# Optimization experiments

Hardware: AMD Instinct MI355X
Metric: run time of the kernel (lower is better)

Reference implementation:

```python
import jax, jax.numpy as jnp
import numpy as np

HIDDEN = 2048
NUM_HEADS = 16
HEAD_DIM = HIDDEN // NUM_HEADS  # 128
SCALE = HEAD_DIM ** -0.5


def setup_inputs() -> dict:
    key = jax.random.key(0)
    ks = jax.random.split(key, 5)
    B, S = 2, 2048
    init = HIDDEN ** -0.5  # roughly kaiming-uniform scale for Linear weights
    return {
        "hidden_states": jax.random.normal(ks[0], (B, S, HIDDEN), dtype=jnp.float32),
        "Wq": jax.random.normal(ks[1], (HIDDEN, HIDDEN), dtype=jnp.float32) * init,
        "Wk": jax.random.normal(ks[2], (HIDDEN, HIDDEN), dtype=jnp.float32) * init,
        "Wv": jax.random.normal(ks[3], (HIDDEN, HIDDEN), dtype=jnp.float32) * init,
        "Wo": jax.random.normal(ks[4], (HIDDEN, HIDDEN), dtype=jnp.float32) * init,
    }


def reference(hidden_states, Wq, Wk, Wv, Wo):
    B, S, _ = hidden_states.shape
    # Projections (nn.Linear: x @ W.T; weights stored as [out, in])
    q = (hidden_states @ Wq.T).reshape(B, S, NUM_HEADS, HEAD_DIM).transpose(0, 2, 1, 3)
    k = (hidden_states @ Wk.T).reshape(B, S, NUM_HEADS, HEAD_DIM).transpose(0, 2, 1, 3)
    v = (hidden_states @ Wv.T).reshape(B, S, NUM_HEADS, HEAD_DIM).transpose(0, 2, 1, 3)
    # Full quadratic attention (faithful to the source's explicit materialization)
    scores = jnp.einsum("bhqd,bhkd->bhqk", q, k) * SCALE  # [B,H,S,S]
    probs = jax.nn.softmax(scores, axis=-1)
    attn = jnp.einsum("bhqk,bhkd->bhqd", probs, v)  # [B,H,S,Dh]
    attn = attn.transpose(0, 2, 1, 3).reshape(B, S, HIDDEN)
    return attn @ Wo.T
```

## Files before the change

### kernel.cpp

```cpp
#include <hip/hip_runtime.h>
#include <cstdint>

#define HIDDEN 2048
#define NHEADS 16
#define DH 128
#define BATCH 2
#define SEQ 2048
#define MTOT 4096
#define BH (BATCH * NHEADS)

typedef __attribute__((ext_vector_type(8))) short bf16x8;
typedef __attribute__((ext_vector_type(4))) float f32x4;

static constexpr float QSCALE = (float)(0.08838834764831845 * 1.4426950408889634);

__device__ __forceinline__ unsigned short f2bf(float f) {
  union { float f; uint32_t u; } v; v.f = f;
  uint32_t r = v.u + 0x7FFFu + ((v.u >> 16) & 1u);
  return (unsigned short)(r >> 16);
}
__device__ __forceinline__ uint32_t cvtpk(float lo, float hi) {
  uint32_t r;
  asm("v_cvt_pk_bf16_f32 %0, %1, %2" : "=v"(r) : "v"(lo), "v"(hi));
  return r;
}
__device__ __forceinline__ f32x4 mfma16(bf16x8 a, bf16x8 b, f32x4 c) {
  return __builtin_amdgcn_mfma_f32_16x16x32_bf16(a, b, c, 0, 0, 0);
}

typedef const __attribute__((address_space(1))) unsigned char* gas1_t;
typedef __attribute__((address_space(3))) unsigned char* las3_t;
__device__ __forceinline__ void gll16(const void* g, void* l) {
  __builtin_amdgcn_global_load_lds((gas1_t)g, (las3_t)l, 16, 0, 0);
}

__global__ __launch_bounds__(256) void cast_all(
    const float* __restrict__ X, const float* __restrict__ Wq,
    const float* __restrict__ Wk, const float* __restrict__ Wv,
    const float* __restrict__ Wo, unsigned short* __restrict__ Xb,
    unsigned short* __restrict__ Wqb, unsigned short* __restrict__ Wkb,
    unsigned short* __restrict__ Wvb, unsigned short* __restrict__ Wob) {
  const int n1 = MTOT * HIDDEN;
  const int i = (blockIdx.x * 256 + threadIdx.x) * 4;
  const float* s;
  unsigned short* d;
  int o;
  if (i < n1) {
    s = X; d = Xb; o = i;
  } else {
    const int j = i - n1;
    const int w = j >> 22;
    o = j & ((1 << 22) - 1);
    s = (w == 0) ? Wq : (w == 1) ? Wk : (w == 2) ? Wv : Wo;
    d = (w == 0) ? Wqb : (w == 1) ? Wkb : (w == 2) ? Wvb : Wob;
  }
  float4 f = *(const float4*)&s[o];
  ushort4 u;
  u.x = f2bf(f.x); u.y = f2bf(f.y); u.z = f2bf(f.z); u.w = f2bf(f.w);
  *(ushort4*)&d[o] = u;
}

template <int VM, bool PF>
__device__ __forceinline__ void pipe_body(
    int kt, char* SM, const unsigned short* aS0, const unsigned short* aS1,
    const unsigned short* bS0, const unsigned short* bS1,
    const unsigned short* bS2, const unsigned short* bS3, int wv, int wr,
    int wc, int g, int lr, f32x4 (&acc)[4][4]) {
  const char* Ac = SM + (kt % 3) * 49152;
  const char* Bc = Ac + 16384;
  char* slot2 = SM + ((kt + 2) % 3) * 49152;
  const size_t ko = (size_t)(kt + 2) * 64;
  const int rx = lr & 7;
  bf16x8 a0[4], b0[4], a1[4], b1[4];
#pragma unroll
  for (int mi = 0; mi < 4; ++mi)
    a0[mi] = *(const bf16x8*)(Ac + (wr * 64 + mi * 16 + lr) * 128 + ((g ^ rx) * 16));
#pragma unroll
  for (int ni = 0; ni < 4; ++ni)
    b0[ni] = *(const bf16x8*)(Bc + (wc * 64 + ni * 16 + lr) * 128 + ((g ^ rx) * 16));
  if (PF) {
    gll16(aS0 + ko, slot2 + wv * 2048);
    gll16(aS1 + ko, slot2 + wv * 2048 + 1024);
    gll16(bS0 + ko, slot2 + 16384 + wv * 4096);
    gll16(bS1 + ko, slot2 + 16384 + wv * 4096 + 1024);
    gll16(bS2 + ko, slot2 + 16384 + wv * 4096 + 2048);
    gll16(bS3 + ko, slot2 + 16384 + wv * 4096 + 3072);
  }
#pragma unroll
  for (int mi = 0; mi < 4; ++mi)
    a1[mi] = *(const bf16x8*)(Ac + (wr * 64 + mi * 16 + lr) * 128 + (((4 + g) ^ rx) * 16));
#pragma unroll
  for (int ni = 0; ni < 4; ++ni)
    b1[ni] = *(const bf16x8*)(Bc + (wc * 64 + ni * 16 + lr) * 128 + (((4 + g) ^ rx) * 16));
  __builtin_amdgcn_s_setprio(1);
#pragma unroll
  for (int mi = 0; mi < 4; ++mi)
#pragma unroll
    for (int ni = 0; ni < 4; ++ni)
      acc[mi][ni] = mfma16(a0[mi], b0[ni], acc[mi][ni]);
#pragma unroll
  for (int mi = 0; mi < 4; ++mi)
#pragma unroll
    for (int ni = 0; ni < 4; ++ni)
      acc[mi][ni] = mfma16(a1[mi], b1[ni], acc[mi][ni]);
  __builtin_amdgcn_s_setprio(0);
  if (VM == 6) asm volatile("s_waitcnt vmcnt(6)" ::: "memory");
  else if (VM == 0) asm volatile("s_waitcnt vmcnt(0)" ::: "memory");
  if (VM >= 0) __builtin_amdgcn_s_barrier();
}

#define PIPE_SETUP(Abase, Bbase)                                              \
  const int idxA0 = wv * 128 + lane, idxA1 = idxA0 + 64;                      \
  const int rA0 = idxA0 >> 3, cA0 = (idxA0 & 7) ^ (rA0 & 7);                  \
  const int rA1 = idxA1 >> 3, cA1 = (idxA1 & 7) ^ (rA1 & 7);                  \
  const unsigned short* aS0 = (Abase) + (size_t)(m0 + rA0) * HIDDEN + cA0 * 8;\
  const unsigned short* aS1 = (Abase) + (size_t)(m0 + rA1) * HIDDEN + cA1 * 8;\
  const int idxB0 = wv * 256 + lane, idxB1 = idxB0 + 64,                      \
            idxB2 = idxB0 + 128, idxB3 = idxB0 + 192;                         \
  const int rB0 = idxB0 >> 3, cB0 = (idxB0 & 7) ^ (rB0 & 7);                  \
  const int rB1 = idxB1 >> 3, cB1 = (idxB1 & 7) ^ (rB1 & 7);                  \
  const int rB2 = idxB2 >> 3, cB2 = (idxB2 & 7) ^ (rB2 & 7);                  \
  const int rB3 = idxB3 >> 3, cB3 = (idxB3 & 7) ^ (rB3 & 7);                  \
  const unsigned short* bS0 = (Bbase) + (size_t)(n0 + rB0) * HIDDEN + cB0 * 8;\
  const unsigned short* bS1 = (Bbase) + (size_t)(n0 + rB1) * HIDDEN + cB1 * 8;\
  const unsigned short* bS2 = (Bbase) + (size_t)(n0 + rB2) * HIDDEN + cB2 * 8;\
  const unsigned short* bS3 = (Bbase) + (size_t)(n0 + rB3) * HIDDEN + cB3 * 8;

#define PIPE_PROLOGUE()                                                       \
  _Pragma("unroll") for (int tt = 0; tt < 2; ++tt) {                          \
    char* slot = SM + tt * 49152;                                             \
    const size_t ko = (size_t)tt * 64;                                        \
    gll16(aS0 + ko, slot + wv * 2048);                                        \
    gll16(aS1 + ko, slot + wv * 2048 + 1024);                                 \
    gll16(bS0 + ko, slot + 16384 + wv * 4096);                                \
    gll16(bS1 + ko, slot + 16384 + wv * 4096 + 1024);                         \
    gll16(bS2 + ko, slot + 16384 + wv * 4096 + 2048);                         \
    gll16(bS3 + ko, slot + 16384 + wv * 4096 + 3072);                         \
  }                                                                           \
  asm volatile("s_waitcnt vmcnt(6)" ::: "memory");                            \
  __builtin_amdgcn_s_barrier();

#define PIPE_LOOP()                                                           \
  for (int kt = 0; kt < 30; ++kt)                                             \
    pipe_body<6, true>(kt, SM, aS0, aS1, bS0, bS1, bS2, bS3, wv, wr, wc, g,   \
                       lr, acc);                                              \
  pipe_body<0, false>(30, SM, aS0, aS1, bS0, bS1, bS2, bS3, wv, wr, wc, g,    \
                      lr, acc);                                               \
  pipe_body<-1, false>(31, SM, aS0, aS1, bS0, bS1, bS2, bS3, wv, wr, wc, g,   \
                       lr, acc);

__global__ __launch_bounds__(512) void gemm_qkv_pipe(
    const unsigned short* __restrict__ A, const unsigned short* __restrict__ Wq,
    const unsigned short* __restrict__ Wk, const unsigned short* __restrict__ Wv,
    unsigned short* __restrict__ Qb, unsigned short* __restrict__ Kb,
    unsigned short* __restrict__ Vb) {
  __shared__ __align__(16) char SM[147456];
  const int tid = threadIdx.x;
  const int lane = tid & 63, wv = tid >> 6;
  const int wr = wv >> 2, wc = wv & 3;
  const int g = lane >> 4, lr = lane & 15;
  const int which = blockIdx.x >> 3;
  const int m0 = blockIdx.y * 128, n0 = (blockIdx.x & 7) * 256;
  const unsigned short* W = (which == 0) ? Wq : (which == 1) ? Wk : Wv;

  PIPE_SETUP(A, W)

  f32x4 acc[4][4];
#pragma unroll
  for (int i = 0; i < 4; ++i)
#pragma unroll
    for (int j = 0; j < 4; ++j) acc[i][j] = (f32x4){0.f, 0.f, 0.f, 0.f};

  PIPE_PROLOGUE()
  PIPE_LOOP()

  const float alpha = (which == 0) ? QSCALE : 1.0f;
  unsigned short* C = (which == 0) ? Qb : (which == 1) ? Kb : Vb;
#pragma unroll
  for (int mi = 0; mi < 4; ++mi)
#pragma unroll
    for (int ni = 0; ni < 4; ++ni)
#pragma unroll
      for (int r = 0; r < 4; ++r) {
        const int row = m0 + wr * 64 + mi * 16 + g * 4 + r;
        const int col = n0 + wc * 64 + ni * 16 + lr;
        const unsigned short v = f2bf(acc[mi][ni][r] * alpha);
        const int b = row >> 11, s = row & (SEQ - 1);
        const int h = col >> 7, d = col & (DH - 1);
        const size_t base = (size_t)(b * NHEADS + h) * SEQ * DH;
        if (which == 0)
          C[base + (size_t)s * DH + d] = v;
        else if (which == 1)
          C[base + (size_t)(s >> 5) * 4096 + (d >> 3) * 256 + (s & 31) * 8 + (d & 7)] = v;
        else
          C[base + (size_t)(s >> 3) * 1024 + d * 8 + (s & 7)] = v;
      }
}

__global__ __launch_bounds__(512) void gemm_out_pipe(
    const unsigned short* __restrict__ A, const unsigned short* __restrict__ W,
    float* __restrict__ C) {
  __shared__ __align__(16) char SM[147456];
  const int tid = threadIdx.x;
  const int lane = tid & 63, wv = tid >> 6;
  const int wr = wv >> 2, wc = wv & 3;
  const int g = lane >> 4, lr = lane & 15;
  const int m0 = blockIdx.y * 128, n0 = blockIdx.x * 256;

  PIPE_SETUP(A, W)

  f32x4 acc[4][4];
#pragma unroll
  for (int i = 0; i < 4; ++i)
#pragma unroll
    for (int j = 0; j < 4; ++j) acc[i][j] = (f32x4){0.f, 0.f, 0.f, 0.f};

  PIPE_PROLOGUE()
  PIPE_LOOP()

#pragma unroll
  for (int mi = 0; mi < 4; ++mi)
#pragma unroll
    for (int ni = 0; ni < 4; ++ni)
#pragma unroll
      for (int r = 0; r < 4; ++r) {
        const int row = m0 + wr * 64 + mi * 16 + g * 4 + r;
        const int col = n0 + wc * 64 + ni * 16 + lr;
        C[(size_t)row * HIDDEN + col] = acc[mi][ni][r];
      }
}

__global__ __launch_bounds__(256, 3) void attn_mfma(const unsigned short* __restrict__ Q,
                                                    const unsigned short* __restrict__ K,
                                                    const unsigned short* __restrict__ V,
                                                    unsigned short* __restrict__ Ab) {
  const int bid = blockIdx.x;
  const int bh = bid & 31;
  const int q0 = (bid >> 5) * 128;
  const int tid = threadIdx.x;
  const int wv = tid >> 6, lane = tid & 63;
  const int g = lane >> 4, lr = lane & 15;
  const unsigned short* Qh = Q + (size_t)bh * SEQ * DH;
  const unsigned short* Kh = K + (size_t)bh * SEQ * DH;
  const unsigned short* Vh = V + (size_t)bh * SEQ * DH;

  __shared__ __align__(16) unsigned short Kls[3][4096];
  __shared__ __align__(16) unsigned short Vls[3][4096];
  __shared__ __align__(16) unsigned short Pw[4][16][40];

  bf16x8 qf[2][4];
#pragma unroll
  for (int m = 0; m < 2; ++m)
#pragma unroll
    for (int kb = 0; kb < 4; ++kb)
      qf[m][kb] = *(const bf16x8*)&Qh[(size_t)(q0 + wv * 32 + m * 16 + lr) * DH +
                                      kb * 32 + g * 8];

  f32x4 acc[2][8];
#pragma unroll
  for (int m = 0; m < 2; ++m)
#pragma unroll
    for (int dn = 0; dn < 8; ++dn) acc[m][dn] = (f32x4){0.f, 0.f, 0.f, 0.f};
  float mrun[2] = {-1e30f, -1e30f};
  float lrun[2] = {0.f, 0.f};

#pragma unroll
  for (int tt = 0; tt < 2; ++tt)
#pragma unroll
    for (int j = 0; j < 2; ++j) {
      const int c = j * 256 + tid;
      gll16(Kh + (size_t)tt * 4096 + c * 8, (char*)&Kls[tt][0] + j * 4096 + wv * 1024);
      gll16(Vh + (size_t)tt * 4096 + c * 8, (char*)&Vls[tt][0] + j * 4096 + wv * 1024);
    }

  for (int t = 0; t < 64; ++t) {
    const int cur = t % 3;
    asm volatile("s_waitcnt vmcnt(4)" ::: "memory");
    __builtin_amdgcn_s_barrier();
    if (t + 2 < 64) {
      const int nx = (t + 2) % 3;
      const unsigned short* Kn = Kh + (size_t)(t + 2) * 4096;
      const unsigned short* Vn = Vh + (size_t)(t + 2) * 4096;
      char* kd = (char*)&Kls[nx][0];
      char* vd = (char*)&Vls[nx][0];
#pragma unroll
      for (int j = 0; j < 2; ++j) {
        const int c = j * 256 + tid;
        gll16(Kn + (size_t)c * 8, kd + j * 4096 + wv * 1024);
        gll16(Vn + (size_t)c * 8, vd + j * 4096 + wv * 1024);
      }
    }

    const char* Kc = (const char*)&Kls[cur][0];
    const char* Vc = (const char*)&Vls[cur][0];
    bf16x8 ap[2];
#pragma unroll
    for (int m = 0; m < 2; ++m) {
      f32x4 st0 = (f32x4){0.f, 0.f, 0.f, 0.f};
      f32x4 st1 = (f32x4){0.f, 0.f, 0.f, 0.f};
      __builtin_amdgcn_s_setprio(1);
#pragma unroll
      for (int kb = 0; kb < 4; ++kb) {
        const int cb = (kb * 4 + g) * 32;
        bf16x8 kf0 = *(const bf16x8*)(Kc + (cb + lr) * 16);
        bf16x8 kf1 = *(const bf16x8*)(Kc + (cb + 16 + lr) * 16);
        st0 = mfma16(kf0, qf[m][kb], st0);
        st1 = mfma16(kf1, qf[m][kb], st1);
      }
      __builtin_amdgcn_s_setprio(0);
      float mt = fmaxf(fmaxf(fmaxf(st0[0], st0[1]), fmaxf(st0[2], st0[3])),
                       fmaxf(fmaxf(st1[0], st1[1]), fmaxf(st1[2], st1[3])));
      mt = fmaxf(mt, __shfl_xor(mt, 16));
      mt = fmaxf(mt, __shfl_xor(mt, 32));
      if (!__all(mt <= mrun[m] + 8.0f)) {
        const float mnew = fmaxf(mrun[m], mt);
        const float corr = __builtin_amdgcn_exp2f(mrun[m] - mnew);
        lrun[m] *= corr;
        mrun[m] = mnew;
        const f32x4 cv = (f32x4){__shfl(corr, g * 4 + 0), __shfl(corr, g * 4 + 1),
                                 __shfl(corr, g * 4 + 2), __shfl(corr, g * 4 + 3)};
#pragma unroll
        for (int dn = 0; dn < 8; ++dn) acc[m][dn] *= cv;
      }
      float p[8], ls = 0.f;
#pragma unroll
      for (int r = 0; r < 4; ++r) {
        p[r] = __builtin_amdgcn_exp2f(st0[r] - mrun[m]);
        p[4 + r] = __builtin_amdgcn_exp2f(st1[r] - mrun[m]);
        ls += p[r] + p[4 + r];
      }
      lrun[m] += ls;
      uint2 pk0, pk1;
      pk0.x = cvtpk(p[0], p[1]); pk0.y = cvtpk(p[2], p[3]);
      pk1.x = cvtpk(p[4], p[5]); pk1.y = cvtpk(p[6], p[7]);
      *(uint2*)&Pw[wv][lr][4 * g] = pk0;
      *(uint2*)&Pw[wv][lr][16 + 4 * g] = pk1;
      ap[m] = *(const bf16x8*)&Pw[wv][lr][8 * g];
    }
    __builtin_amdgcn_s_setprio(1);
#pragma unroll
    for (int dn = 0; dn < 8; ++dn) {
      bf16x8 vf = *(const bf16x8*)(Vc + (g * 128 + dn * 16 + lr) * 16);
      acc[0][dn] = mfma16(ap[0], vf, acc[0][dn]);
      acc[1][dn] = mfma16(ap[1], vf, acc[1][dn]);
    }
    __builtin_amdgcn_s_setprio(0);
  }

  const int b = bh >> 4, h = bh & 15;
#pragma unroll
  for (int m = 0; m < 2; ++m) {
    lrun[m] += __shfl_xor(lrun[m], 16);
    lrun[m] += __shfl_xor(lrun[m], 32);
    const float inv = 1.f / lrun[m];
    float ir[4];
#pragma unroll
    for (int r = 0; r < 4; ++r) ir[r] = __shfl(inv, g * 4 + r);
#pragma unroll
    for (int dn = 0; dn < 8; ++dn)
#pragma unroll
      for (int r = 0; r < 4; ++r) {
        const int srow = q0 + wv * 32 + m * 16 + g * 4 + r;
        Ab[((size_t)(b * SEQ + srow) * NHEADS + h) * DH + dn * 16 + lr] =
            f2bf(acc[m][dn][r] * ir[r]);
      }
  }
}

extern "C" void kernel_launch(void* const* d_in, const int* in_sizes, int n_in,
                              void* d_out, int out_size, void* d_ws,
                              size_t ws_size, hipStream_t stream) {
  const float* X  = (const float*)d_in[0];
  const float* Wq = (const float*)d_in[1];
  const float* Wk = (const float*)d_in[2];
  const float* Wv = (const float*)d_in[3];
  const float* Wo = (const float*)d_in[4];
  float* out = (float*)d_out;

  const int n1 = MTOT * HIDDEN;
  const int n2 = HIDDEN * HIDDEN;

  char* p = (char*)d_ws;
  unsigned short* Xb  = (unsigned short*)(p + 0);
  unsigned short* Qb  = (unsigned short*)(p + 16777216);
  unsigned short* Kb  = (unsigned short*)(p + 33554432);
  unsigned short* Vb  = (unsigned short*)(p + 50331648);
  unsigned short* Wqb = (unsigned short*)(p + 67108864);
  unsigned short* Wkb = (unsigned short*)(p + 75497472);
  unsigned short* Wvb = (unsigned short*)(p + 83886080);
  unsigned short* Wob = (unsigned short*)(p + 92274688);
  unsigned short* Ab  = (unsigned short*)(p + 100663296);

  cast_all<<<(n1 + 4 * n2) / 1024, 256, 0, stream>>>(X, Wq, Wk, Wv, Wo, Xb, Wqb,
                                                     Wkb, Wvb, Wob);

  gemm_qkv_pipe<<<dim3(24, MTOT / 128), 512, 0, stream>>>(Xb, Wqb, Wkb, Wvb,
                                                          Qb, Kb, Vb);

  attn_mfma<<<dim3(512), 256, 0, stream>>>(Qb, Kb, Vb, Ab);

  gemm_out_pipe<<<dim3(HIDDEN / 256, MTOT / 128), 512, 0, stream>>>(Ab, Wob, out);
}
```

Baseline: 270.4 us.

## Split GEMM k-step into four interleaved load/MFMA phases with barriers

Restructures the pipelined GEMM inner step into four smaller phases. Each phase loads two A fragments (plus B fragments when needed), issues part of the global prefetch, and runs eight MFMAs, with workgroup barriers between phases. This cuts register pressure from holding all A/B fragments at once and aims to interleave LDS reads, global loads and MFMA work across waves, in the style of ping-pong scheduling. In exchange it adds seven extra barriers per k-step, which may stall waves.

```diff
diff --git a/kernel.cpp b/kernel.cpp
--- a/kernel.cpp
+++ b/kernel.cpp
@@ -71,38 +71,72 @@
   char* slot2 = SM + ((kt + 2) % 3) * 49152;
   const size_t ko = (size_t)(kt + 2) * 64;
   const int rx = lr & 7;
-  bf16x8 a0[4], b0[4], a1[4], b1[4];
-#pragma unroll
-  for (int mi = 0; mi < 4; ++mi)
-    a0[mi] = *(const bf16x8*)(Ac + (wr * 64 + mi * 16 + lr) * 128 + ((g ^ rx) * 16));
+  const int c0 = (g ^ rx) * 16, c1 = ((4 + g) ^ rx) * 16;
+  bf16x8 a0, a1, b[4];
+
+  a0 = *(const bf16x8*)(Ac + (wr * 64 + 0 * 16 + lr) * 128 + c0);
+  a1 = *(const bf16x8*)(Ac + (wr * 64 + 1 * 16 + lr) * 128 + c0);
 #pragma unroll
   for (int ni = 0; ni < 4; ++ni)
-    b0[ni] = *(const bf16x8*)(Bc + (wc * 64 + ni * 16 + lr) * 128 + ((g ^ rx) * 16));
+    b[ni] = *(const bf16x8*)(Bc + (wc * 64 + ni * 16 + lr) * 128 + c0);
   if (PF) {
     gll16(aS0 + ko, slot2 + wv * 2048);
     gll16(aS1 + ko, slot2 + wv * 2048 + 1024);
+  }
+  __builtin_amdgcn_s_barrier();
+  __builtin_amdgcn_s_setprio(1);
+#pragma unroll
+  for (int ni = 0; ni < 4; ++ni) {
+    acc[0][ni] = mfma16(a0, b[ni], acc[0][ni]);
+    acc[1][ni] = mfma16(a1, b[ni], acc[1][ni]);
+  }
+  __builtin_amdgcn_s_setprio(0);
+  __builtin_amdgcn_s_barrier();
+
+  a0 = *(const bf16x8*)(Ac + (wr * 64 + 2 * 16 + lr) * 128 + c0);
+  a1 = *(const bf16x8*)(Ac + (wr * 64 + 3 * 16 + lr) * 128 + c0);
+  if (PF) {
     gll16(bS0 + ko, slot2 + 16384 + wv * 4096);
     gll16(bS1 + ko, slot2 + 16384 + wv * 4096 + 1024);
+  }
+  __builtin_amdgcn_s_barrier();
+  __builtin_amdgcn_s_setprio(1);
+#pragma unroll
+  for (int ni = 0; ni < 4; ++ni) {
+    acc[2][ni] = mfma16(a0, b[ni], acc[2][ni]);
+    acc[3][ni] = mfma16(a1, b[ni], acc[3][ni]);
+  }
+  __builtin_amdgcn_s_setprio(0);
+  __builtin_amdgcn_s_barrier();
+
+  a0 = *(const bf16x8*)(Ac + (wr * 64 + 0 * 16 + lr) * 128 + c1);
+  a1 = *(const bf16x8*)(Ac + (wr * 64 + 1 * 16 + lr) * 128 + c1);
+#pragma unroll
+  for (int ni = 0; ni < 4; ++ni)
+    b[ni] = *(const bf16x8*)(Bc + (wc * 64 + ni * 16 + lr) * 128 + c1);
+  if (PF) {
     gll16(bS2 + ko, slot2 + 16384 + wv * 4096 + 2048);
     gll16(bS3 + ko, slot2 + 16384 + wv * 4096 + 3072);
   }
-#pragma unroll
-  for (int mi = 0; mi < 4; ++mi)
-    a1[mi] = *(const bf16x8*)(Ac + (wr * 64 + mi * 16 + lr) * 128 + (((4 + g) ^ rx) * 16));
-#pragma unroll
-  for (int ni = 0; ni < 4; ++ni)
-    b1[ni] = *(const bf16x8*)(Bc + (wc * 64 + ni * 16 + lr) * 128 + (((4 + g) ^ rx) * 16));
+  __builtin_amdgcn_s_barrier();
   __builtin_amdgcn_s_setprio(1);
 #pragma unroll
-  for (int mi = 0; mi < 4; ++mi)
-#pragma unroll
-    for (int ni = 0; ni < 4; ++ni)
-      acc[mi][ni] = mfma16(a0[mi], b0[ni], acc[mi][ni]);
-#pragma unroll
-  for (int mi = 0; mi < 4; ++mi)
-#pragma unroll
-    for (int ni = 0; ni < 4; ++ni)
-      acc[mi][ni] = mfma16(a1[mi], b1[ni], acc[mi][ni]);
+  for (int ni = 0; ni < 4; ++ni) {
+    acc[0][ni] = mfma16(a0, b[ni], acc[0][ni]);
+    acc[1][ni] = mfma16(a1, b[ni], acc[1][ni]);
+  }
+  __builtin_amdgcn_s_setprio(0);
+  __builtin_amdgcn_s_barrier();
+
+  a0 = *(const bf16x8*)(Ac + (wr * 64 + 2 * 16 + lr) * 128 + c1);
+  a1 = *(const bf16x8*)(Ac + (wr * 64 + 3 * 16 + lr) * 128 + c1);
+  __builtin_amdgcn_s_barrier();
+  __builtin_amdgcn_s_setprio(1);
+#pragma unroll
+  for (int ni = 0; ni < 4; ++ni) {
+    acc[2][ni] = mfma16(a0, b[ni], acc[2][ni]);
+    acc[3][ni] = mfma16(a1, b[ni], acc[3][ni]);
+  }
   __builtin_amdgcn_s_setprio(0);
   if (VM == 6) asm volatile("s_waitcnt vmcnt(6)" ::: "memory");
   else if (VM == 0) asm volatile("s_waitcnt vmcnt(0)" ::: "memory");
```

After: 271.8 us. About the same (+0.6%).

## Halve attention query tile to 64 rows and use double-buffered K/V

Applied to the files above, without the earlier changes.

Each attention block now handles 64 query rows instead of 128, so each wave owns one 16-row tile and the grid grows from 512 to 1024 blocks. The K/V LDS ring drops from triple to double buffering with a full vmcnt(0) wait, and launch bounds rise to 4 blocks per CU. The goal is more parallelism and occupancy with lower register and LDS use. In exchange, K/V traffic from global memory doubles because each tile is reused by fewer queries, and the shallower prefetch exposes more load latency.

```diff
diff --git a/kernel.cpp b/kernel.cpp
--- a/kernel.cpp
+++ b/kernel.cpp
@@ -230,13 +230,13 @@
       }
 }
 
-__global__ __launch_bounds__(256, 3) void attn_mfma(const unsigned short* __restrict__ Q,
+__global__ __launch_bounds__(256, 4) void attn_mfma(const unsigned short* __restrict__ Q,
                                                     const unsigned short* __restrict__ K,
                                                     const unsigned short* __restrict__ V,
                                                     unsigned short* __restrict__ Ab) {
   const int bid = blockIdx.x;
   const int bh = bid & 31;
-  const int q0 = (bid >> 5) * 128;
+  const int q0 = (bid >> 5) * 64;
   const int tid = threadIdx.x;
   const int wv = tid >> 6, lane = tid & 63;
   const int g = lane >> 4, lr = lane & 15;
@@ -244,45 +244,37 @@
   const unsigned short* Kh = K + (size_t)bh * SEQ * DH;
   const unsigned short* Vh = V + (size_t)bh * SEQ * DH;
 
-  __shared__ __align__(16) unsigned short Kls[3][4096];
-  __shared__ __align__(16) unsigned short Vls[3][4096];
+  __shared__ __align__(16) unsigned short Kls[2][4096];
+  __shared__ __align__(16) unsigned short Vls[2][4096];
   __shared__ __align__(16) unsigned short Pw[4][16][40];
 
-  bf16x8 qf[2][4];
-#pragma unroll
-  for (int m = 0; m < 2; ++m)
-#pragma unroll
-    for (int kb = 0; kb < 4; ++kb)
-      qf[m][kb] = *(const bf16x8*)&Qh[(size_t)(q0 + wv * 32 + m * 16 + lr) * DH +
-                                      kb * 32 + g * 8];
-
-  f32x4 acc[2][8];
-#pragma unroll
-  for (int m = 0; m < 2; ++m)
-#pragma unroll
-    for (int dn = 0; dn < 8; ++dn) acc[m][dn] = (f32x4){0.f, 0.f, 0.f, 0.f};
-  float mrun[2] = {-1e30f, -1e30f};
-  float lrun[2] = {0.f, 0.f};
-
-#pragma unroll
-  for (int tt = 0; tt < 2; ++tt)
-#pragma unroll
-    for (int j = 0; j < 2; ++j) {
-      const int c = j * 256 + tid;
-      gll16(Kh + (size_t)tt * 4096 + c * 8, (char*)&Kls[tt][0] + j * 4096 + wv * 1024);
-      gll16(Vh + (size_t)tt * 4096 + c * 8, (char*)&Vls[tt][0] + j * 4096 + wv * 1024);
-    }
+  bf16x8 qf[4];
+#pragma unroll
+  for (int kb = 0; kb < 4; ++kb)
+    qf[kb] = *(const bf16x8*)&Qh[(size_t)(q0 + wv * 16 + lr) * DH + kb * 32 + g * 8];
+
+  f32x4 acc[8];
+#pragma unroll
+  for (int dn = 0; dn < 8; ++dn) acc[dn] = (f32x4){0.f, 0.f, 0.f, 0.f};
+  float mrun = -1e30f;
+  float lrun = 0.f;
+
+#pragma unroll
+  for (int j = 0; j < 2; ++j) {
+    const int c = j * 256 + tid;
+    gll16(Kh + (size_t)c * 8, (char*)&Kls[0][0] + j * 4096 + wv * 1024);
+    gll16(Vh + (size_t)c * 8, (char*)&Vls[0][0] + j * 4096 + wv * 1024);
+  }
 
   for (int t = 0; t < 64; ++t) {
-    const int cur = t % 3;
-    asm volatile("s_waitcnt vmcnt(4)" ::: "memory");
+    const int cur = t & 1;
+    asm volatile("s_waitcnt vmcnt(0)" ::: "memory");
     __builtin_amdgcn_s_barrier();
-    if (t + 2 < 64) {
-      const int nx = (t + 2) % 3;
-      const unsigned short* Kn = Kh + (size_t)(t + 2) * 4096;
-      const unsigned short* Vn = Vh + (size_t)(t + 2) * 4096;
-      char* kd = (char*)&Kls[nx][0];
-      char* vd = (char*)&Vls[nx][0];
+    if (t + 1 < 64) {
+      const unsigned short* Kn = Kh + (size_t)(t + 1) * 4096;
+      const unsigned short* Vn = Vh + (size_t)(t + 1) * 4096;
+      char* kd = (char*)&Kls[cur ^ 1][0];
+      char* vd = (char*)&Vls[cur ^ 1][0];
 #pragma unroll
       for (int j = 0; j < 2; ++j) {
         const int c = j * 256 + tid;
@@ -293,78 +285,71 @@
 
     const char* Kc = (const char*)&Kls[cur][0];
     const char* Vc = (const char*)&Vls[cur][0];
-    bf16x8 ap[2];
-#pragma unroll
-    for (int m = 0; m < 2; ++m) {
-      f32x4 st0 = (f32x4){0.f, 0.f, 0.f, 0.f};
-      f32x4 st1 = (f32x4){0.f, 0.f, 0.f, 0.f};
-      __builtin_amdgcn_s_setprio(1);
-#pragma unroll
-      for (int kb = 0; kb < 4; ++kb) {
-        const int cb = (kb * 4 + g) * 32;
-        bf16x8 kf0 = *(const bf16x8*)(Kc + (cb + lr) * 16);
-        bf16x8 kf1 = *(const bf16x8*)(Kc + (cb + 16 + lr) * 16);
-        st0 = mfma16(kf0, qf[m][kb], st0);
-        st1 = mfma16(kf1, qf[m][kb], st1);
-      }
-      __builtin_amdgcn_s_setprio(0);
-      float mt = fmaxf(fmaxf(fmaxf(st0[0], st0[1]), fmaxf(st0[2], st0[3])),
-                       fmaxf(fmaxf(st1[0], st1[1]), fmaxf(st1[2], st1[3])));
-      mt = fmaxf(mt, __shfl_xor(mt, 16));
-      mt = fmaxf(mt, __shfl_xor(mt, 32));
-      if (!__all(mt <= mrun[m] + 8.0f)) {
-        const float mnew = fmaxf(mrun[m], mt);
-        const float corr = __builtin_amdgcn_exp2f(mrun[m] - mnew);
-        lrun[m] *= corr;
-        mrun[m] = mnew;
-        const f32x4 cv = (f32x4){__shfl(corr, g * 4 + 0), __shfl(corr, g * 4 + 1),
-                                 __shfl(corr, g * 4 + 2), __shfl(corr, g * 4 + 3)};
-#pragma unroll
-        for (int dn = 0; dn < 8; ++dn) acc[m][dn] *= cv;
-      }
-      float p[8], ls = 0.f;
-#pragma unroll
-      for (int r = 0; r < 4; ++r) {
-        p[r] = __builtin_amdgcn_exp2f(st0[r] - mrun[m]);
-        p[4 + r] = __builtin_amdgcn_exp2f(st1[r] - mrun[m]);
-        ls += p[r] + p[4 + r];
-      }
-      lrun[m] += ls;
-      uint2 pk0, pk1;
-      pk0.x = cvtpk(p[0], p[1]); pk0.y = cvtpk(p[2], p[3]);
-      pk1.x = cvtpk(p[4], p[5]); pk1.y = cvtpk(p[6], p[7]);
-      *(uint2*)&Pw[wv][lr][4 * g] = pk0;
-      *(uint2*)&Pw[wv][lr][16 + 4 * g] = pk1;
-      ap[m] = *(const bf16x8*)&Pw[wv][lr][8 * g];
-    }
+
+    f32x4 st0 = (f32x4){0.f, 0.f, 0.f, 0.f};
+    f32x4 st1 = (f32x4){0.f, 0.f, 0.f, 0.f};
+    __builtin_amdgcn_s_setprio(1);
+#pragma unroll
+    for (int kb = 0; kb < 4; ++kb) {
+      const int cb = (kb * 4 + g) * 32;
+      bf16x8 kf0 = *(const bf16x8*)(Kc + (cb + lr) * 16);
+      bf16x8 kf1 = *(const bf16x8*)(Kc + (cb + 16 + lr) * 16);
+      st0 = mfma16(kf0, qf[kb], st0);
+      st1 = mfma16(kf1, qf[kb], st1);
+    }
+    __builtin_amdgcn_s_setprio(0);
+    float mt = fmaxf(fmaxf(fmaxf(st0[0], st0[1]), fmaxf(st0[2], st0[3])),
+                     fmaxf(fmaxf(st1[0], st1[1]), fmaxf(st1[2], st1[3])));
+    mt = fmaxf(mt, __shfl_xor(mt, 16));
+    mt = fmaxf(mt, __shfl_xor(mt, 32));
+    if (!__all(mt <= mrun + 8.0f)) {
+      const float mnew = fmaxf(mrun, mt);
+      const float corr = __builtin_amdgcn_exp2f(mrun - mnew);
+      lrun *= corr;
+      mrun = mnew;
+      const f32x4 cv = (f32x4){__shfl(corr, g * 4 + 0), __shfl(corr, g * 4 + 1),
+                               __shfl(corr, g * 4 + 2), __shfl(corr, g * 4 + 3)};
+#pragma unroll
+      for (int dn = 0; dn < 8; ++dn) acc[dn] *= cv;
+    }
+    float p[8], ls = 0.f;
+#pragma unroll
+    for (int r = 0; r < 4; ++r) {
+      p[r] = __builtin_amdgcn_exp2f(st0[r] - mrun);
+      p[4 + r] = __builtin_amdgcn_exp2f(st1[r] - mrun);
+      ls += p[r] + p[4 + r];
+    }
+    lrun += ls;
+    uint2 pk0, pk1;
+    pk0.x = cvtpk(p[0], p[1]); pk0.y = cvtpk(p[2], p[3]);
+    pk1.x = cvtpk(p[4], p[5]); pk1.y = cvtpk(p[6], p[7]);
+    *(uint2*)&Pw[wv][lr][4 * g] = pk0;
+    *(uint2*)&Pw[wv][lr][16 + 4 * g] = pk1;
+    bf16x8 ap = *(const bf16x8*)&Pw[wv][lr][8 * g];
     __builtin_amdgcn_s_setprio(1);
 #pragma unroll
     for (int dn = 0; dn < 8; ++dn) {
       bf16x8 vf = *(const bf16x8*)(Vc + (g * 128 + dn * 16 + lr) * 16);
-      acc[0][dn] = mfma16(ap[0], vf, acc[0][dn]);
-      acc[1][dn] = mfma16(ap[1], vf, acc[1][dn]);
+      acc[dn] = mfma16(ap, vf, acc[dn]);
     }
     __builtin_amdgcn_s_setprio(0);
   }
 
   const int b = bh >> 4, h = bh & 15;
-#pragma unroll
-  for (int m = 0; m < 2; ++m) {
-    lrun[m] += __shfl_xor(lrun[m], 16);
-    lrun[m] += __shfl_xor(lrun[m], 32);
-    const float inv = 1.f / lrun[m];
-    float ir[4];
-#pragma unroll
-    for (int r = 0; r < 4; ++r) ir[r] = __shfl(inv, g * 4 + r);
-#pragma unroll
-    for (int dn = 0; dn < 8; ++dn)
-#pragma unroll
-      for (int r = 0; r < 4; ++r) {
-        const int srow = q0 + wv * 32 + m * 16 + g * 4 + r;
-        Ab[((size_t)(b * SEQ + srow) * NHEADS + h) * DH + dn * 16 + lr] =
-            f2bf(acc[m][dn][r] * ir[r]);
-      }
-  }
+  lrun += __shfl_xor(lrun, 16);
+  lrun += __shfl_xor(lrun, 32);
+  const float inv = 1.f / lrun;
+  float ir[4];
+#pragma unroll
+  for (int r = 0; r < 4; ++r) ir[r] = __shfl(inv, g * 4 + r);
+#pragma unroll
+  for (int dn = 0; dn < 8; ++dn)
+#pragma unroll
+    for (int r = 0; r < 4; ++r) {
+      const int srow = q0 + wv * 16 + g * 4 + r;
+      Ab[((size_t)(b * SEQ + srow) * NHEADS + h) * DH + dn * 16 + lr] =
+          f2bf(acc[dn][r] * ir[r]);
+    }
 }
 
 extern "C" void kernel_launch(void* const* d_in, const int* in_sizes, int n_in,
@@ -397,7 +382,7 @@
   gemm_qkv_pipe<<<dim3(24, MTOT / 128), 512, 0, stream>>>(Xb, Wqb, Wkb, Wvb,
                                                           Qb, Kb, Vb);
 
-  attn_mfma<<<dim3(512), 256, 0, stream>>>(Qb, Kb, Vb, Ab);
+  attn_mfma<<<dim3(1024), 256, 0, stream>>>(Qb, Kb, Vb, Ab);
 
   gemm_out_pipe<<<dim3(HIDDEN / 256, MTOT / 128), 512, 0, stream>>>(Ab, Wob, out);
 }
```

Result: no change. 269.2 us (median of 4 runs) (-0.4%).
